# Performance work log

Measured on AMD Instinct MI355X. Metric: run time of the kernel, lower is better.

Reference implementation:

```python
import jax, jax.numpy as jnp
import numpy as np

P, B, C, H, W = 8, 8, 64, 32, 32


def setup_inputs() -> dict:
    key = jax.random.key(0)
    k1, k2, k3 = jax.random.split(key, 3)
    shape = (P, B, C, H, W)
    return {
        "K_set": jax.random.normal(k1, shape, dtype=jnp.float32),
        "J_set": jax.random.normal(k2, shape, dtype=jnp.float32),
        "V_set": jax.random.normal(k3, shape, dtype=jnp.float32),
    }


def reference(K_set, J_set, V_set):
    # K_set/J_set/V_set: [P, B, C, H, W]; N = H*W spatial tokens.
    p, b, c, h, w = K_set.shape
    n = h * w
    Kf = K_set.reshape(p, b, c, n)  # [P,B,C,N]
    Jf = J_set.reshape(p, b, c, n)  # [P,B,C,N] (original permutes to [B,N,C])
    Vf = V_set.reshape(p, b, c, n)  # [P,B,C,N]
    # scores[p,b,j,k] = sum_c J[p,b,c,j] * K[p,b,c,k]  (unscaled QK^T)
    scores = jnp.einsum('pbcj,pbck->pbjk', Jf, Kf)
    # Original: F.softmax(bmm(J_pie, K_pie), dim=1) -> softmax over the J-token axis (j)
    att = jax.nn.softmax(scores, axis=2)
    # out[p,b,c,k] = sum_j V[p,b,c,j] * att[p,b,j,k]
    out = jnp.einsum('pbcj,pbjk->pbck', Vf, att)
    return out.reshape(p, b, c, h, w)
```

## Files before the change

### kernel.cpp

```cpp
#include <hip/hip_runtime.h>


typedef short bf16x8 __attribute__((ext_vector_type(8)));
typedef short bf16x4 __attribute__((ext_vector_type(4)));
typedef float f32x4  __attribute__((ext_vector_type(4)));

#define NTOK 1024
#define CH   64
#define KTW  128
#define JTILE 32
#define KW   32
#define SJK  72
#define SV   40

__device__ __forceinline__ unsigned short f2bf_rne(float x) {
  unsigned int u = __float_as_uint(x);
  u += 0x7FFFu + ((u >> 16) & 1u);
  return (unsigned short)(u >> 16);
}

#define MFMA(a, b, c) __builtin_amdgcn_mfma_f32_16x16x32_bf16((a), (b), (c), 0, 0, 0)

__global__ __launch_bounds__(256, 2) void attn_v2(
    const float* __restrict__ Kg, const float* __restrict__ Jg,
    const float* __restrict__ Vg, float* __restrict__ Og) {
  __shared__ unsigned short KhS[KTW][SJK];
  __shared__ unsigned short KlS[KTW][SJK];
  __shared__ unsigned short JhS[JTILE][SJK];
  __shared__ unsigned short JlS[JTILE][SJK];
  __shared__ unsigned short VtS[CH][SV];
  __shared__ unsigned short PtS[4][KW][SV];

  const int tid  = threadIdx.x;
  const int lane = tid & 63;
  const int wave = tid >> 6;
  const int l15  = lane & 15;
  const int l4   = lane >> 4;

  const int bid   = blockIdx.x;
  const int batch = bid & 63;
  const int ktile = bid >> 6;
  const int k0    = ktile * KTW;
  const size_t base = (size_t)batch * (CH * NTOK);

  const float* Kp = Kg + base;
  const float* Jp = Jg + base;
  const float* Vp = Vg + base;
  float*       Op = Og + base;

  #pragma unroll
  for (int i = 0; i < 4; ++i) {
    int task = i * 256 + tid;
    int k    = task & (KTW - 1);
    int oct  = task >> 7;
    const float* src = Kp + (size_t)(oct * 8) * NTOK + k0 + k;
    bf16x8 hv, lv;
    #pragma unroll
    for (int r = 0; r < 8; ++r) {
      float v = src[(size_t)r * NTOK];
      unsigned int u = __float_as_uint(v);
      hv[r] = (short)(u >> 16);
      float hf = __uint_as_float(u & 0xFFFF0000u);
      lv[r] = (short)(__float_as_uint(v - hf) >> 16);
    }
    *(bf16x8*)&KhS[k][oct * 8] = hv;
    *(bf16x8*)&KlS[k][oct * 8] = lv;
  }
  __syncthreads();

  bf16x8 kbh[2][2], kbl[2][2];
  #pragma unroll
  for (int ks = 0; ks < 2; ++ks) {
    #pragma unroll
    for (int cd = 0; cd < 2; ++cd) {
      kbh[ks][cd] = *(const bf16x8*)&KhS[wave * KW + ks * 16 + l15][cd * 32 + l4 * 8];
      kbl[ks][cd] = *(const bf16x8*)&KlS[wave * KW + ks * 16 + l15][cd * 32 + l4 * 8];
    }
  }

  const int jJ   = tid & 31;
  const int octJ = tid >> 5;
  const float* srcJ = Jp + (size_t)(octJ * 8) * NTOK + jJ;
  const int c0  = tid >> 3;
  const int jq0 = tid & 7;
  const float* srcV = Vp + (size_t)c0 * NTOK + jq0 * 4;

  f32x4 U[4][2];
  #pragma unroll
  for (int a = 0; a < 4; ++a) {
    #pragma unroll
    for (int b = 0; b < 2; ++b) U[a][b] = (f32x4){0.f, 0.f, 0.f, 0.f};
  }
  float zacc0 = 0.f, zacc1 = 0.f;

  auto issue_loads = [&](float (&jr)[8], float4 (&vr)[2], int j0) {
    #pragma unroll
    for (int r = 0; r < 8; ++r) jr[r] = srcJ[(size_t)r * NTOK + j0];
    vr[0] = *(const float4*)(srcV + j0);
    vr[1] = *(const float4*)(srcV + (size_t)32 * NTOK + j0);
  };

  auto stage = [&](float (&jr)[8], float4 (&vr)[2]) {
    bf16x8 hv, lv;
    #pragma unroll
    for (int r = 0; r < 8; ++r) {
      unsigned int u = __float_as_uint(jr[r]);
      hv[r] = (short)(u >> 16);
      float hf = __uint_as_float(u & 0xFFFF0000u);
      lv[r] = (short)(__float_as_uint(jr[r] - hf) >> 16);
    }
    *(bf16x8*)&JhS[jJ][octJ * 8] = hv;
    *(bf16x8*)&JlS[jJ][octJ * 8] = lv;
    bf16x4 w0, w1;
    w0[0] = (short)f2bf_rne(vr[0].x); w0[1] = (short)f2bf_rne(vr[0].y);
    w0[2] = (short)f2bf_rne(vr[0].z); w0[3] = (short)f2bf_rne(vr[0].w);
    w1[0] = (short)f2bf_rne(vr[1].x); w1[1] = (short)f2bf_rne(vr[1].y);
    w1[2] = (short)f2bf_rne(vr[1].z); w1[3] = (short)f2bf_rne(vr[1].w);
    *(bf16x4*)&VtS[c0][jq0 * 4]      = w0;
    *(bf16x4*)&VtS[c0 + 32][jq0 * 4] = w1;
  };

  auto compute = [&]() {
    f32x4 S[2][2];
    #pragma unroll
    for (int a = 0; a < 2; ++a) {
      #pragma unroll
      for (int b = 0; b < 2; ++b) S[a][b] = (f32x4){0.f, 0.f, 0.f, 0.f};
    }
    #pragma unroll
    for (int cd = 0; cd < 2; ++cd) {
      const int co = cd * 32 + l4 * 8;
      bf16x8 ah0 = *(const bf16x8*)&JhS[l15][co];
      bf16x8 ah1 = *(const bf16x8*)&JhS[l15 + 16][co];
      bf16x8 al0 = *(const bf16x8*)&JlS[l15][co];
      bf16x8 al1 = *(const bf16x8*)&JlS[l15 + 16][co];
      #pragma unroll
      for (int ks = 0; ks < 2; ++ks) {
        S[0][ks] = MFMA(ah0, kbh[ks][cd], S[0][ks]);
        S[0][ks] = MFMA(ah0, kbl[ks][cd], S[0][ks]);
        S[0][ks] = MFMA(al0, kbh[ks][cd], S[0][ks]);
        S[1][ks] = MFMA(ah1, kbh[ks][cd], S[1][ks]);
        S[1][ks] = MFMA(ah1, kbl[ks][cd], S[1][ks]);
        S[1][ks] = MFMA(al1, kbh[ks][cd], S[1][ks]);
      }
    }
    #pragma unroll
    for (int js = 0; js < 2; ++js) {
      #pragma unroll
      for (int ks = 0; ks < 2; ++ks) {
        f32x4 s = S[js][ks];
        float e0 = __expf(s[0]);
        float e1 = __expf(s[1]);
        float e2 = __expf(s[2]);
        float e3 = __expf(s[3]);
        if (ks == 0) zacc0 += (e0 + e1) + (e2 + e3);
        else         zacc1 += (e0 + e1) + (e2 + e3);
        bf16x4 pv;
        pv[0] = (short)f2bf_rne(e0); pv[1] = (short)f2bf_rne(e1);
        pv[2] = (short)f2bf_rne(e2); pv[3] = (short)f2bf_rne(e3);
        *(bf16x4*)&PtS[wave][l15 + ks * 16][js * 16 + l4 * 4] = pv;
      }
    }
    bf16x8 pb0 = *(const bf16x8*)&PtS[wave][l15][l4 * 8];
    bf16x8 pb1 = *(const bf16x8*)&PtS[wave][l15 + 16][l4 * 8];
    #pragma unroll
    for (int ct = 0; ct < 4; ++ct) {
      bf16x8 av = *(const bf16x8*)&VtS[ct * 16 + l15][l4 * 8];
      U[ct][0] = MFMA(av, pb0, U[ct][0]);
      U[ct][1] = MFMA(av, pb1, U[ct][1]);
    }
  };

  float jrA[8], jrB[8];
  float4 vrA[2], vrB[2];
  issue_loads(jrA, vrA, 0);

  #pragma unroll 1
  for (int pr = 0; pr < NTOK / JTILE / 2; ++pr) {
    __syncthreads();
    stage(jrA, vrA);
    __syncthreads();
    issue_loads(jrB, vrB, (2 * pr + 1) * JTILE);
    compute();

    __syncthreads();
    stage(jrB, vrB);
    __syncthreads();
    {
      int jn = (2 * pr + 2 < NTOK / JTILE) ? (2 * pr + 2) * JTILE : 0;
      issue_loads(jrA, vrA, jn);
    }
    compute();
  }

  float z0 = zacc0; z0 += __shfl_xor(z0, 16); z0 += __shfl_xor(z0, 32);
  float z1 = zacc1; z1 += __shfl_xor(z1, 16); z1 += __shfl_xor(z1, 32);
  const float rz0 = 1.0f / z0;
  const float rz1 = 1.0f / z1;
  const int kbase = k0 + wave * KW;
  #pragma unroll
  for (int ct = 0; ct < 4; ++ct) {
    #pragma unroll
    for (int r = 0; r < 4; ++r) {
      int c = ct * 16 + l4 * 4 + r;
      Op[(size_t)c * NTOK + kbase + l15]      = U[ct][0][r] * rz0;
      Op[(size_t)c * NTOK + kbase + 16 + l15] = U[ct][1][r] * rz1;
    }
  }
}

extern "C" void kernel_launch(void* const* d_in, const int* in_sizes, int n_in,
                              void* d_out, int out_size, void* d_ws, size_t ws_size,
                              hipStream_t stream) {
  const float* Kg = (const float*)d_in[0];
  const float* Jg = (const float*)d_in[1];
  const float* Vg = (const float*)d_in[2];
  float* Og = (float*)d_out;
  attn_v2<<<dim3(512), dim3(256), 0, stream>>>(Kg, Jg, Vg, Og);
}
```

Before: 124.5 us.

## Split J-axis across waves with smaller K tiles and LDS reduction

Halves the K tile per block to 64 and doubles the grid to 1024 blocks. Inside a block, waves are arranged 2x2: two split the K columns and two split each 64-token J tile, and the J-split partial outputs and softmax denominators are combined through LDS at the end. The shared buffer is reused between the K staging, J, V and P regions, occupancy is raised to 4 blocks per CU, and s_setprio is added around the MFMA sections. The J/V prefetch is reduced to a single register set that is issued after the barrier. The aim is more parallelism and fewer barriers per token, in exchange for an extra reduction step, more redundant J/V loads across blocks, and a less deep prefetch.

```diff
diff --git a/kernel.cpp b/kernel.cpp
--- a/kernel.cpp
+++ b/kernel.cpp
@@ -7,11 +7,11 @@
 
 #define NTOK 1024
 #define CH   64
-#define KTW  128
-#define JTILE 32
-#define KW   32
+#define KTW  64
+#define JTILE 64
+#define NIT  (NTOK / JTILE)
 #define SJK  72
-#define SV   40
+#define SP   40
 
 __device__ __forceinline__ unsigned short f2bf_rne(float x) {
   unsigned int u = __float_as_uint(x);
@@ -19,41 +19,91 @@
   return (unsigned short)(u >> 16);
 }
 
-#define MFMA(a, b, c) __builtin_amdgcn_mfma_f32_16x16x32_bf16((a), (b), (c), 0, 0, 0)
-
-__global__ __launch_bounds__(256, 2) void attn_v2(
+#define MFMA(a,b,c) __builtin_amdgcn_mfma_f32_16x16x32_bf16((a),(b),(c),0,0,0)
+
+__global__ __launch_bounds__(256, 4) void attn_v3(
     const float* __restrict__ Kg, const float* __restrict__ Jg,
     const float* __restrict__ Vg, float* __restrict__ Og) {
-  __shared__ unsigned short KhS[KTW][SJK];
-  __shared__ unsigned short KlS[KTW][SJK];
-  __shared__ unsigned short JhS[JTILE][SJK];
-  __shared__ unsigned short JlS[JTILE][SJK];
-  __shared__ unsigned short VtS[CH][SV];
-  __shared__ unsigned short PtS[4][KW][SV];
+  __shared__ __align__(16) unsigned char LDSBUF[37888];
+  unsigned short (*KhS)[SJK] = (unsigned short (*)[SJK])(LDSBUF);
+  unsigned short (*KlS)[SJK] = (unsigned short (*)[SJK])(LDSBUF + 9216);
+  unsigned short (*JhS)[SJK] = (unsigned short (*)[SJK])(LDSBUF);
+  unsigned short (*JlS)[SJK] = (unsigned short (*)[SJK])(LDSBUF + 9216);
+  unsigned short (*VtS)[SJK] = (unsigned short (*)[SJK])(LDSBUF + 18432);
 
   const int tid  = threadIdx.x;
   const int lane = tid & 63;
   const int wave = tid >> 6;
+  const int wk   = wave & 1;
+  const int wj   = wave >> 1;
   const int l15  = lane & 15;
   const int l4   = lane >> 4;
+
+  unsigned short (*PtS)[SP] = (unsigned short (*)[SP])(LDSBUF + 27648 + wave * 2560);
 
   const int bid   = blockIdx.x;
   const int batch = bid & 63;
   const int ktile = bid >> 6;
   const int k0    = ktile * KTW;
   const size_t base = (size_t)batch * (CH * NTOK);
-
   const float* Kp = Kg + base;
   const float* Jp = Jg + base;
   const float* Vp = Vg + base;
   float*       Op = Og + base;
 
+  const int jJ   = tid & 63;
+  const int octJ = tid >> 6;
+  const float* srcJ = Jp + (size_t)(octJ * 8) * NTOK + jJ;
+  const int c0v = tid >> 2;
+  const int jc0 = (tid & 3) * 16;
+  const float* srcV = Vp + (size_t)c0v * NTOK + jc0;
+
+  float  jr[2][8];
+  float4 vr[4];
+
+  auto issueJ = [&](int j0) {
+    #pragma unroll
+    for (int t = 0; t < 2; ++t)
+      #pragma unroll
+      for (int r = 0; r < 8; ++r)
+        jr[t][r] = srcJ[(size_t)(t * 32 + r) * NTOK + j0];
+  };
+  auto issueV = [&](int j0) {
+    #pragma unroll
+    for (int q = 0; q < 4; ++q)
+      vr[q] = *(const float4*)(srcV + j0 + q * 4);
+  };
+  auto stageJ = [&]() {
+    #pragma unroll
+    for (int t = 0; t < 2; ++t) {
+      bf16x8 hv, lv;
+      #pragma unroll
+      for (int r = 0; r < 8; ++r) {
+        unsigned int u = __float_as_uint(jr[t][r]);
+        hv[r] = (short)(u >> 16);
+        float hf = __uint_as_float(u & 0xFFFF0000u);
+        lv[r] = (short)(__float_as_uint(jr[t][r] - hf) >> 16);
+      }
+      *(bf16x8*)&JhS[jJ][(octJ + 4 * t) * 8] = hv;
+      *(bf16x8*)&JlS[jJ][(octJ + 4 * t) * 8] = lv;
+    }
+  };
+  auto stageV = [&]() {
+    #pragma unroll
+    for (int q = 0; q < 4; ++q) {
+      bf16x4 w;
+      w[0] = (short)f2bf_rne(vr[q].x); w[1] = (short)f2bf_rne(vr[q].y);
+      w[2] = (short)f2bf_rne(vr[q].z); w[3] = (short)f2bf_rne(vr[q].w);
+      *(bf16x4*)&VtS[c0v][jc0 + q * 4] = w;
+    }
+  };
+
+  issueJ(0);
+  issueV(0);
+
   #pragma unroll
-  for (int i = 0; i < 4; ++i) {
-    int task = i * 256 + tid;
-    int k    = task & (KTW - 1);
-    int oct  = task >> 7;
-    const float* src = Kp + (size_t)(oct * 8) * NTOK + k0 + k;
+  for (int t = 0; t < 2; ++t) {
+    const float* src = Kp + (size_t)((octJ + 4 * t) * 8) * NTOK + k0 + jJ;
     bf16x8 hv, lv;
     #pragma unroll
     for (int r = 0; r < 8; ++r) {
@@ -63,77 +113,49 @@
       float hf = __uint_as_float(u & 0xFFFF0000u);
       lv[r] = (short)(__float_as_uint(v - hf) >> 16);
     }
-    *(bf16x8*)&KhS[k][oct * 8] = hv;
-    *(bf16x8*)&KlS[k][oct * 8] = lv;
+    *(bf16x8*)&KhS[jJ][(octJ + 4 * t) * 8] = hv;
+    *(bf16x8*)&KlS[jJ][(octJ + 4 * t) * 8] = lv;
   }
   __syncthreads();
 
   bf16x8 kbh[2][2], kbl[2][2];
   #pragma unroll
-  for (int ks = 0; ks < 2; ++ks) {
+  for (int ks = 0; ks < 2; ++ks)
     #pragma unroll
     for (int cd = 0; cd < 2; ++cd) {
-      kbh[ks][cd] = *(const bf16x8*)&KhS[wave * KW + ks * 16 + l15][cd * 32 + l4 * 8];
-      kbl[ks][cd] = *(const bf16x8*)&KlS[wave * KW + ks * 16 + l15][cd * 32 + l4 * 8];
-    }
-  }
-
-  const int jJ   = tid & 31;
-  const int octJ = tid >> 5;
-  const float* srcJ = Jp + (size_t)(octJ * 8) * NTOK + jJ;
-  const int c0  = tid >> 3;
-  const int jq0 = tid & 7;
-  const float* srcV = Vp + (size_t)c0 * NTOK + jq0 * 4;
+      kbh[ks][cd] = *(const bf16x8*)&KhS[wk * 32 + ks * 16 + l15][cd * 32 + l4 * 8];
+      kbl[ks][cd] = *(const bf16x8*)&KlS[wk * 32 + ks * 16 + l15][cd * 32 + l4 * 8];
+      asm volatile("" : "+v"(kbh[ks][cd]), "+v"(kbl[ks][cd]));
+    }
+  __syncthreads();
 
   f32x4 U[4][2];
   #pragma unroll
-  for (int a = 0; a < 4; ++a) {
+  for (int a = 0; a < 4; ++a)
     #pragma unroll
     for (int b = 0; b < 2; ++b) U[a][b] = (f32x4){0.f, 0.f, 0.f, 0.f};
-  }
   float zacc0 = 0.f, zacc1 = 0.f;
 
-  auto issue_loads = [&](float (&jr)[8], float4 (&vr)[2], int j0) {
-    #pragma unroll
-    for (int r = 0; r < 8; ++r) jr[r] = srcJ[(size_t)r * NTOK + j0];
-    vr[0] = *(const float4*)(srcV + j0);
-    vr[1] = *(const float4*)(srcV + (size_t)32 * NTOK + j0);
-  };
-
-  auto stage = [&](float (&jr)[8], float4 (&vr)[2]) {
-    bf16x8 hv, lv;
-    #pragma unroll
-    for (int r = 0; r < 8; ++r) {
-      unsigned int u = __float_as_uint(jr[r]);
-      hv[r] = (short)(u >> 16);
-      float hf = __uint_as_float(u & 0xFFFF0000u);
-      lv[r] = (short)(__float_as_uint(jr[r] - hf) >> 16);
-    }
-    *(bf16x8*)&JhS[jJ][octJ * 8] = hv;
-    *(bf16x8*)&JlS[jJ][octJ * 8] = lv;
-    bf16x4 w0, w1;
-    w0[0] = (short)f2bf_rne(vr[0].x); w0[1] = (short)f2bf_rne(vr[0].y);
-    w0[2] = (short)f2bf_rne(vr[0].z); w0[3] = (short)f2bf_rne(vr[0].w);
-    w1[0] = (short)f2bf_rne(vr[1].x); w1[1] = (short)f2bf_rne(vr[1].y);
-    w1[2] = (short)f2bf_rne(vr[1].z); w1[3] = (short)f2bf_rne(vr[1].w);
-    *(bf16x4*)&VtS[c0][jq0 * 4]      = w0;
-    *(bf16x4*)&VtS[c0 + 32][jq0 * 4] = w1;
-  };
-
-  auto compute = [&]() {
+  #pragma unroll 1
+  for (int it = 0; it < NIT; ++it) {
+    stageJ();
+    stageV();
+    __syncthreads();
+    if (it + 1 < NIT) issueJ((it + 1) * JTILE);
+
     f32x4 S[2][2];
     #pragma unroll
-    for (int a = 0; a < 2; ++a) {
+    for (int a = 0; a < 2; ++a)
       #pragma unroll
       for (int b = 0; b < 2; ++b) S[a][b] = (f32x4){0.f, 0.f, 0.f, 0.f};
-    }
+    __builtin_amdgcn_s_setprio(1);
     #pragma unroll
     for (int cd = 0; cd < 2; ++cd) {
       const int co = cd * 32 + l4 * 8;
-      bf16x8 ah0 = *(const bf16x8*)&JhS[l15][co];
-      bf16x8 ah1 = *(const bf16x8*)&JhS[l15 + 16][co];
-      bf16x8 al0 = *(const bf16x8*)&JlS[l15][co];
-      bf16x8 al1 = *(const bf16x8*)&JlS[l15 + 16][co];
+      bf16x8 ah0 = *(const bf16x8*)&JhS[wj * 32 + l15][co];
+      bf16x8 ah1 = *(const bf16x8*)&JhS[wj * 32 + 16 + l15][co];
+      bf16x8 al0 = *(const bf16x8*)&JlS[wj * 32 + l15][co];
+      bf16x8 al1 = *(const bf16x8*)&JlS[wj * 32 + 16 + l15][co];
       #pragma unroll
       for (int ks = 0; ks < 2; ++ks) {
         S[0][ks] = MFMA(ah0, kbh[ks][cd], S[0][ks]);
@@ -144,8 +166,10 @@
         S[1][ks] = MFMA(al1, kbh[ks][cd], S[1][ks]);
       }
     }
-    #pragma unroll
-    for (int js = 0; js < 2; ++js) {
+    __builtin_amdgcn_s_setprio(0);
+
+    #pragma unroll
+    for (int js = 0; js < 2; ++js)
       #pragma unroll
       for (int ks = 0; ks < 2; ++ks) {
         f32x4 s = S[js][ks];
@@ -158,54 +182,58 @@
         bf16x4 pv;
         pv[0] = (short)f2bf_rne(e0); pv[1] = (short)f2bf_rne(e1);
         pv[2] = (short)f2bf_rne(e2); pv[3] = (short)f2bf_rne(e3);
-        *(bf16x4*)&PtS[wave][l15 + ks * 16][js * 16 + l4 * 4] = pv;
+        *(bf16x4*)&PtS[ks * 16 + l15][js * 16 + l4 * 4] = pv;
       }
-    }
-    bf16x8 pb0 = *(const bf16x8*)&PtS[wave][l15][l4 * 8];
-    bf16x8 pb1 = *(const bf16x8*)&PtS[wave][l15 + 16][l4 * 8];
+
+    if (it + 1 < NIT) issueV((it + 1) * JTILE);
+
+    bf16x8 pb0 = *(const bf16x8*)&PtS[l15][l4 * 8];
+    bf16x8 pb1 = *(const bf16x8*)&PtS[16 + l15][l4 * 8];
+    __builtin_amdgcn_s_setprio(1);
     #pragma unroll
     for (int ct = 0; ct < 4; ++ct) {
-      bf16x8 av = *(const bf16x8*)&VtS[ct * 16 + l15][l4 * 8];
+      bf16x8 av = *(const bf16x8*)&VtS[ct * 16 + l15][wj * 32 + l4 * 8];
       U[ct][0] = MFMA(av, pb0, U[ct][0]);
       U[ct][1] = MFMA(av, pb1, U[ct][1]);
     }
-  };
-
-  float jrA[8], jrB[8];
-  float4 vrA[2], vrB[2];
-  issue_loads(jrA, vrA, 0);
-
-  #pragma unroll 1
-  for (int pr = 0; pr < NTOK / JTILE / 2; ++pr) {
+    __builtin_amdgcn_s_setprio(0);
     __syncthreads();
-    stage(jrA, vrA);
-    __syncthreads();
-    issue_loads(jrB, vrB, (2 * pr + 1) * JTILE);
-    compute();
-
-    __syncthreads();
-    stage(jrB, vrB);
-    __syncthreads();
-    {
-      int jn = (2 * pr + 2 < NTOK / JTILE) ? (2 * pr + 2) * JTILE : 0;
-      issue_loads(jrA, vrA, jn);
-    }
-    compute();
   }
 
   float z0 = zacc0; z0 += __shfl_xor(z0, 16); z0 += __shfl_xor(z0, 32);
   float z1 = zacc1; z1 += __shfl_xor(z1, 16); z1 += __shfl_xor(z1, 32);
-  const float rz0 = 1.0f / z0;
-  const float rz1 = 1.0f / z1;
-  const int kbase = k0 + wave * KW;
-  #pragma unroll
-  for (int ct = 0; ct < 4; ++ct) {
-    #pragma unroll
-    for (int r = 0; r < 4; ++r) {
-      int c = ct * 16 + l4 * 4 + r;
-      Op[(size_t)c * NTOK + kbase + l15]      = U[ct][0][r] * rz0;
-      Op[(size_t)c * NTOK + kbase + 16 + l15] = U[ct][1][r] * rz1;
-    }
+
+  float* UL = (float*)(LDSBUF);
+  float* ZL = (float*)(LDSBUF + 16384);
+  if (wj == 1) {
+    #pragma unroll
+    for (int ct = 0; ct < 4; ++ct)
+      #pragma unroll
+      for (int ks = 0; ks < 2; ++ks)
+        #pragma unroll
+        for (int r = 0; r < 4; ++r)
+          UL[((size_t)wk * 64 + ct * 16 + l4 * 4 + r) * 32 + ks * 16 + l15] = U[ct][ks][r];
+    if (lane < 16) {
+      ZL[wk * 32 + l15]      = z0;
+      ZL[wk * 32 + 16 + l15] = z1;
+    }
+  }
+  __syncthreads();
+  if (wj == 0) {
+    z0 += ZL[wk * 32 + l15];
+    z1 += ZL[wk * 32 + 16 + l15];
+    const float rz0 = 1.0f / z0;
+    const float rz1 = 1.0f / z1;
+    #pragma unroll
+    for (int ct = 0; ct < 4; ++ct)
+      #pragma unroll
+      for (int ks = 0; ks < 2; ++ks)
+        #pragma unroll
+        for (int r = 0; r < 4; ++r) {
+          const int c = ct * 16 + l4 * 4 + r;
+          float u = U[ct][ks][r] + UL[((size_t)wk * 64 + c) * 32 + ks * 16 + l15];
+          Op[(size_t)c * NTOK + k0 + wk * 32 + ks * 16 + l15] = u * (ks ? rz1 : rz0);
+        }
   }
 }
 
@@ -216,5 +244,5 @@
   const float* Jg = (const float*)d_in[1];
   const float* Vg = (const float*)d_in[2];
   float* Og = (float*)d_out;
-  attn_v2<<<dim3(512), dim3(256), 0, stream>>>(Kg, Jg, Vg, Og);
+  attn_v3<<<dim3(1024), dim3(256), 0, stream>>>(Kg, Jg, Vg, Og);
 }
```

New measurement: 163.2 us. 1.31x slower.

## Double-buffer J/V shared tiles with one barrier per iteration and MFMA priority

Applied to the files above, without the earlier changes.

Moves the J and V tiles into double-buffered shared memory, so the next tile is staged into the other buffer after compute and each iteration needs one barrier instead of two. Starts the first J/V global load before the K preload, sets wave priority around the MFMA blocks, and changes shared-memory padding strides. The goal is to cut barrier stalls and hide global load latency, at the cost of more LDS per block, which could lower occupancy.

```diff
diff --git a/kernel.cpp b/kernel.cpp
--- a/kernel.cpp
+++ b/kernel.cpp
@@ -9,9 +9,10 @@
 #define CH   64
 #define KTW  128
 #define JTILE 32
-#define KW   32
-#define SJK  72
-#define SV   40
+#define NIT  (NTOK / JTILE)
+#define SJK  76
+#define SV   36
+#define SP   36
 
 __device__ __forceinline__ unsigned short f2bf_rne(float x) {
   unsigned int u = __float_as_uint(x);
@@ -19,17 +20,17 @@
   return (unsigned short)(u >> 16);
 }
 
-#define MFMA(a, b, c) __builtin_amdgcn_mfma_f32_16x16x32_bf16((a), (b), (c), 0, 0, 0)
-
-__global__ __launch_bounds__(256, 2) void attn_v2(
+#define MFMA(a,b,c) __builtin_amdgcn_mfma_f32_16x16x32_bf16((a),(b),(c),0,0,0)
+
+__global__ __launch_bounds__(256, 2) void attn_v4(
     const float* __restrict__ Kg, const float* __restrict__ Jg,
     const float* __restrict__ Vg, float* __restrict__ Og) {
   __shared__ unsigned short KhS[KTW][SJK];
   __shared__ unsigned short KlS[KTW][SJK];
-  __shared__ unsigned short JhS[JTILE][SJK];
-  __shared__ unsigned short JlS[JTILE][SJK];
-  __shared__ unsigned short VtS[CH][SV];
-  __shared__ unsigned short PtS[4][KW][SV];
+  __shared__ unsigned short JhS[2][JTILE][SJK];
+  __shared__ unsigned short JlS[2][JTILE][SJK];
+  __shared__ unsigned short VtS[2][CH][SV];
+  __shared__ unsigned short PtS[4][JTILE][SP];
 
   const int tid  = threadIdx.x;
   const int lane = tid & 63;
@@ -42,11 +43,48 @@
   const int ktile = bid >> 6;
   const int k0    = ktile * KTW;
   const size_t base = (size_t)batch * (CH * NTOK);
-
   const float* Kp = Kg + base;
   const float* Jp = Jg + base;
   const float* Vp = Vg + base;
   float*       Op = Og + base;
+
+  const int jJ   = tid & 31;
+  const int octJ = tid >> 5;
+  const float* srcJ = Jp + (size_t)(octJ * 8) * NTOK + jJ;
+  const int c0  = tid >> 3;
+  const int jq0 = tid & 7;
+  const float* srcV = Vp + (size_t)c0 * NTOK + jq0 * 4;
+
+  float  jr[8];
+  float4 vr[2];
+
+  auto issueJV = [&](int j0) {
+    #pragma unroll
+    for (int r = 0; r < 8; ++r) jr[r] = srcJ[(size_t)r * NTOK + j0];
+    vr[0] = *(const float4*)(srcV + j0);
+    vr[1] = *(const float4*)(srcV + (size_t)32 * NTOK + j0);
+  };
+  auto stageJV = [&](int buf) {
+    bf16x8 hv, lv;
+    #pragma unroll
+    for (int r = 0; r < 8; ++r) {
+      unsigned int u = __float_as_uint(jr[r]);
+      hv[r] = (short)(u >> 16);
+      float hf = __uint_as_float(u & 0xFFFF0000u);
+      lv[r] = (short)(__float_as_uint(jr[r] - hf) >> 16);
+    }
+    *(bf16x8*)&JhS[buf][jJ][octJ * 8] = hv;
+    *(bf16x8*)&JlS[buf][jJ][octJ * 8] = lv;
+    bf16x4 w0, w1;
+    w0[0] = (short)f2bf_rne(vr[0].x); w0[1] = (short)f2bf_rne(vr[0].y);
+    w0[2] = (short)f2bf_rne(vr[0].z); w0[3] = (short)f2bf_rne(vr[0].w);
+    w1[0] = (short)f2bf_rne(vr[1].x); w1[1] = (short)f2bf_rne(vr[1].y);
+    w1[2] = (short)f2bf_rne(vr[1].z); w1[3] = (short)f2bf_rne(vr[1].w);
+    *(bf16x4*)&VtS[buf][c0][jq0 * 4]      = w0;
+    *(bf16x4*)&VtS[buf][c0 + 32][jq0 * 4] = w1;
+  };
+
+  issueJV(0);
 
   #pragma unroll
   for (int i = 0; i < 4; ++i) {
@@ -70,70 +108,42 @@
 
   bf16x8 kbh[2][2], kbl[2][2];
   #pragma unroll
-  for (int ks = 0; ks < 2; ++ks) {
+  for (int ks = 0; ks < 2; ++ks)
     #pragma unroll
     for (int cd = 0; cd < 2; ++cd) {
-      kbh[ks][cd] = *(const bf16x8*)&KhS[wave * KW + ks * 16 + l15][cd * 32 + l4 * 8];
-      kbl[ks][cd] = *(const bf16x8*)&KlS[wave * KW + ks * 16 + l15][cd * 32 + l4 * 8];
-    }
-  }
-
-  const int jJ   = tid & 31;
-  const int octJ = tid >> 5;
-  const float* srcJ = Jp + (size_t)(octJ * 8) * NTOK + jJ;
-  const int c0  = tid >> 3;
-  const int jq0 = tid & 7;
-  const float* srcV = Vp + (size_t)c0 * NTOK + jq0 * 4;
+      kbh[ks][cd] = *(const bf16x8*)&KhS[wave * 32 + ks * 16 + l15][cd * 32 + l4 * 8];
+      kbl[ks][cd] = *(const bf16x8*)&KlS[wave * 32 + ks * 16 + l15][cd * 32 + l4 * 8];
+      asm volatile("" : "+v"(kbh[ks][cd]), "+v"(kbl[ks][cd]));
+    }
+
+  stageJV(0);
+  __syncthreads();
 
   f32x4 U[4][2];
   #pragma unroll
-  for (int a = 0; a < 4; ++a) {
+  for (int a = 0; a < 4; ++a)
     #pragma unroll
     for (int b = 0; b < 2; ++b) U[a][b] = (f32x4){0.f, 0.f, 0.f, 0.f};
-  }
   float zacc0 = 0.f, zacc1 = 0.f;
 
-  auto issue_loads = [&](float (&jr)[8], float4 (&vr)[2], int j0) {
-    #pragma unroll
-    for (int r = 0; r < 8; ++r) jr[r] = srcJ[(size_t)r * NTOK + j0];
-    vr[0] = *(const float4*)(srcV + j0);
-    vr[1] = *(const float4*)(srcV + (size_t)32 * NTOK + j0);
-  };
-
-  auto stage = [&](float (&jr)[8], float4 (&vr)[2]) {
-    bf16x8 hv, lv;
-    #pragma unroll
-    for (int r = 0; r < 8; ++r) {
-      unsigned int u = __float_as_uint(jr[r]);
-      hv[r] = (short)(u >> 16);
-      float hf = __uint_as_float(u & 0xFFFF0000u);
-      lv[r] = (short)(__float_as_uint(jr[r] - hf) >> 16);
-    }
-    *(bf16x8*)&JhS[jJ][octJ * 8] = hv;
-    *(bf16x8*)&JlS[jJ][octJ * 8] = lv;
-    bf16x4 w0, w1;
-    w0[0] = (short)f2bf_rne(vr[0].x); w0[1] = (short)f2bf_rne(vr[0].y);
-    w0[2] = (short)f2bf_rne(vr[0].z); w0[3] = (short)f2bf_rne(vr[0].w);
-    w1[0] = (short)f2bf_rne(vr[1].x); w1[1] = (short)f2bf_rne(vr[1].y);
-    w1[2] = (short)f2bf_rne(vr[1].z); w1[3] = (short)f2bf_rne(vr[1].w);
-    *(bf16x4*)&VtS[c0][jq0 * 4]      = w0;
-    *(bf16x4*)&VtS[c0 + 32][jq0 * 4] = w1;
-  };
-
-  auto compute = [&]() {
+  int cur = 0;
+  #pragma unroll 1
+  for (int it = 0; it < NIT; ++it) {
+    if (it + 1 < NIT) issueJV((it + 1) * JTILE);
+
     f32x4 S[2][2];
     #pragma unroll
-    for (int a = 0; a < 2; ++a) {
+    for (int a = 0; a < 2; ++a)
       #pragma unroll
       for (int b = 0; b < 2; ++b) S[a][b] = (f32x4){0.f, 0.f, 0.f, 0.f};
-    }
+    __builtin_amdgcn_s_setprio(1);
     #pragma unroll
     for (int cd = 0; cd < 2; ++cd) {
       const int co = cd * 32 + l4 * 8;
-      bf16x8 ah0 = *(const bf16x8*)&JhS[l15][co];
-      bf16x8 ah1 = *(const bf16x8*)&JhS[l15 + 16][co];
-      bf16x8 al0 = *(const bf16x8*)&JlS[l15][co];
-      bf16x8 al1 = *(const bf16x8*)&JlS[l15 + 16][co];
+      bf16x8 ah0 = *(const bf16x8*)&JhS[cur][l15][co];
+      bf16x8 ah1 = *(const bf16x8*)&JhS[cur][l15 + 16][co];
+      bf16x8 al0 = *(const bf16x8*)&JlS[cur][l15][co];
+      bf16x8 al1 = *(const bf16x8*)&JlS[cur][l15 + 16][co];
       #pragma unroll
       for (int ks = 0; ks < 2; ++ks) {
         S[0][ks] = MFMA(ah0, kbh[ks][cd], S[0][ks]);
@@ -144,8 +154,10 @@
         S[1][ks] = MFMA(al1, kbh[ks][cd], S[1][ks]);
       }
     }
-    #pragma unroll
-    for (int js = 0; js < 2; ++js) {
+    __builtin_amdgcn_s_setprio(0);
+
+    #pragma unroll
+    for (int js = 0; js < 2; ++js)
       #pragma unroll
       for (int ks = 0; ks < 2; ++ks) {
         f32x4 s = S[js][ks];
@@ -158,55 +170,38 @@
         bf16x4 pv;
         pv[0] = (short)f2bf_rne(e0); pv[1] = (short)f2bf_rne(e1);
         pv[2] = (short)f2bf_rne(e2); pv[3] = (short)f2bf_rne(e3);
-        *(bf16x4*)&PtS[wave][l15 + ks * 16][js * 16 + l4 * 4] = pv;
+        *(bf16x4*)&PtS[wave][ks * 16 + l15][js * 16 + l4 * 4] = pv;
       }
-    }
+
     bf16x8 pb0 = *(const bf16x8*)&PtS[wave][l15][l4 * 8];
-    bf16x8 pb1 = *(const bf16x8*)&PtS[wave][l15 + 16][l4 * 8];
+    bf16x8 pb1 = *(const bf16x8*)&PtS[wave][16 + l15][l4 * 8];
+    __builtin_amdgcn_s_setprio(1);
     #pragma unroll
     for (int ct = 0; ct < 4; ++ct) {
-      bf16x8 av = *(const bf16x8*)&VtS[ct * 16 + l15][l4 * 8];
+      bf16x8 av = *(const bf16x8*)&VtS[cur][ct * 16 + l15][l4 * 8];
       U[ct][0] = MFMA(av, pb0, U[ct][0]);
       U[ct][1] = MFMA(av, pb1, U[ct][1]);
     }
-  };
-
-  float jrA[8], jrB[8];
-  float4 vrA[2], vrB[2];
-  issue_loads(jrA, vrA, 0);
-
-  #pragma unroll 1
-  for (int pr = 0; pr < NTOK / JTILE / 2; ++pr) {
+    __builtin_amdgcn_s_setprio(0);
+
+    if (it + 1 < NIT) stageJV(cur ^ 1);
     __syncthreads();
-    stage(jrA, vrA);
-    __syncthreads();
-    issue_loads(jrB, vrB, (2 * pr + 1) * JTILE);
-    compute();
-
-    __syncthreads();
-    stage(jrB, vrB);
-    __syncthreads();
-    {
-      int jn = (2 * pr + 2 < NTOK / JTILE) ? (2 * pr + 2) * JTILE : 0;
-      issue_loads(jrA, vrA, jn);
-    }
-    compute();
+    cur ^= 1;
   }
 
   float z0 = zacc0; z0 += __shfl_xor(z0, 16); z0 += __shfl_xor(z0, 32);
   float z1 = zacc1; z1 += __shfl_xor(z1, 16); z1 += __shfl_xor(z1, 32);
   const float rz0 = 1.0f / z0;
   const float rz1 = 1.0f / z1;
-  const int kbase = k0 + wave * KW;
-  #pragma unroll
-  for (int ct = 0; ct < 4; ++ct) {
+  const int kbase = k0 + wave * 32;
+  #pragma unroll
+  for (int ct = 0; ct < 4; ++ct)
     #pragma unroll
     for (int r = 0; r < 4; ++r) {
       int c = ct * 16 + l4 * 4 + r;
       Op[(size_t)c * NTOK + kbase + l15]      = U[ct][0][r] * rz0;
       Op[(size_t)c * NTOK + kbase + 16 + l15] = U[ct][1][r] * rz1;
     }
-  }
 }
 
 extern "C" void kernel_launch(void* const* d_in, const int* in_sizes, int n_in,
@@ -216,5 +211,5 @@
   const float* Jg = (const float*)d_in[1];
   const float* Vg = (const float*)d_in[2];
   float* Og = (float*)d_out;
-  attn_v2<<<dim3(512), dim3(256), 0, stream>>>(Kg, Jg, Vg, Og);
+  attn_v4<<<dim3(512), dim3(256), 0, stream>>>(Kg, Jg, Vg, Og);
 }
```

Result: no change. 125.7 us (+1.0%).
